# Kernel optimization log

Hardware: AMD Instinct MI355X
Metric: run time of the kernel (lower is better)

Reference implementation:

```python
import jax, jax.numpy as jnp
import numpy as np

EPS = 1e-5
ALPHA = 0.05   # propalpha
GDEP = 2       # gcn_depth
LAYERS = 3     # gcn_layers
NUM_TCN = 2    # num_layer tcn units per encoder


def conv1x1(W, b, x):
    # 1x1 Conv2d on [B,C,N,1]: pure channel mix
    return jnp.einsum('oc,bcnl->bonl', W, x) + b[None, :, None, None]


def tcn_unit(Wf, bf, Wg, bg, h):
    # gated TCN unit: tanh(filter) * sigmoid(gate), 1x1 convs (L==1)
    return jnp.tanh(conv1x1(Wf, bf, h)) * jax.nn.sigmoid(conv1x1(Wg, bg, h))


def mixprop(x, A, W, b):
    # MTGNN mixprop: add self-loops, row-normalize, gdep propagation steps,
    # concat hops on channel dim, 1x1 conv mlp. A: [N,N] or [B,N,N].
    N = A.shape[-1]
    A = A + jnp.eye(N, dtype=A.dtype)
    A = A / A.sum(-1, keepdims=True)
    h = x
    outs = [h]
    for _ in range(GDEP):
        if A.ndim == 2:
            hn = jnp.einsum('vw,bcwl->bcvl', A, h)
        else:
            hn = jnp.einsum('bvw,bcwl->bcvl', A, h)
        h = ALPHA * x + (1.0 - ALPHA) * hn
        outs.append(h)
    ho = jnp.concatenate(outs, axis=1)  # [B,(GDEP+1)*C,N,1]
    return conv1x1(W, b, ho)


def layernorm(x, w, b):
    # LayerNorm over (C,N,1) of [B,C,N,1]; idx=arange(N) selects full affine
    mu = x.mean(axis=(1, 2, 3), keepdims=True)
    var = x.var(axis=(1, 2, 3), keepdims=True)
    return (x - mu) / jnp.sqrt(var + EPS) * w[None] + b[None]


def setup_inputs() -> dict:
    key = jax.random.key(0)
    B, N, E, H, S, T = 8, 2048, 32, 128, 256, 12
    ks = jax.random.split(key, 32)
    s = 0.05
    inp = {
        'x': jax.random.normal(ks[0], (B, E, N, 1), jnp.float32),
        'dy_graph': jax.random.uniform(ks[1], (B, N, N), jnp.float32),
        'static_graph': jax.random.uniform(ks[2], (N, N), jnp.float32),
        'spatial_emb': jax.random.normal(ks[3], (B, 32, N, 1), jnp.float32),
        'temporal_d_emb': jax.random.normal(ks[4], (B, 32, N, 1), jnp.float32),
        'temporal_w_emb': jax.random.normal(ks[5], (B, 32, N, 1), jnp.float32),
        'enc_Wf': s * jax.random.normal(ks[6], (LAYERS, NUM_TCN, H, H), jnp.float32),
        'enc_bf': s * jax.random.normal(ks[7], (LAYERS, NUM_TCN, H), jnp.float32),
        'enc_Wg': s * jax.random.normal(ks[8], (LAYERS, NUM_TCN, H, H), jnp.float32),
        'enc_bg': s * jax.random.normal(ks[9], (LAYERS, NUM_TCN, H), jnp.float32),
        'skip_W': s * jax.random.normal(ks[10], (LAYERS, S, H), jnp.float32),
        'skip_b': s * jax.random.normal(ks[11], (LAYERS, S), jnp.float32),
        'norm_w': jnp.ones((LAYERS, E, N, 1), jnp.float32),
        'norm_b': jnp.zeros((LAYERS, E, N, 1), jnp.float32),
        'g0_W': s * jax.random.normal(ks[12], (LAYERS, E, (GDEP + 1) * E), jnp.float32),
        'g0_b': s * jax.random.normal(ks[13], (LAYERS, E), jnp.float32),
        'g1_W': s * jax.random.normal(ks[14], (LAYERS, E, (GDEP + 1) * E), jnp.float32),
        'g1_b': s * jax.random.normal(ks[15], (LAYERS, E), jnp.float32),
        'g2_W': s * jax.random.normal(ks[16], (LAYERS, E, (GDEP + 1) * E), jnp.float32),
        'g2_b': s * jax.random.normal(ks[17], (LAYERS, E), jnp.float32),
        'skipE_W': s * jax.random.normal(ks[18], (S, E), jnp.float32),
        'skipE_b': s * jax.random.normal(ks[19], (S,), jnp.float32),
        'end_W': s * jax.random.normal(ks[20], (T, S), jnp.float32),
        'end_b': s * jax.random.normal(ks[21], (T,), jnp.float32),
    }
    return inp


def reference(x, dy_graph, static_graph, spatial_emb, temporal_d_emb, temporal_w_emb,
              enc_Wf, enc_bf, enc_Wg, enc_bg, skip_W, skip_b, norm_w, norm_b,
              g0_W, g0_b, g1_W, g1_b, g2_W, g2_b, skipE_W, skipE_b, end_W, end_b):
    adp = dy_graph
    skip = 0.0
    for i in range(LAYERS):
        residual = x
        hidden = jnp.concatenate([x, spatial_emb, temporal_d_emb, temporal_w_emb], axis=1)
        for j in range(NUM_TCN):
            hidden = tcn_unit(enc_Wf[i, j], enc_bf[i, j], enc_Wg[i, j], enc_bg[i, j], hidden)
        skip = conv1x1(skip_W[i], skip_b[i], hidden) + skip
        x = (mixprop(x, static_graph, g0_W[i], g0_b[i])
             + mixprop(x, adp, g1_W[i], g1_b[i])
             + mixprop(x, jnp.swapaxes(adp, -1, -2), g2_W[i], g2_b[i]))
        x = x + residual
        x = jax.nn.relu(layernorm(x, norm_w[i], norm_b[i]))
    skip = conv1x1(skipE_W, skipE_b, x) + skip
    return conv1x1(end_W, end_b, skip)  # [B, seq_length, N, 1]
```

## Files before the change

### kernel.cpp

```cpp
#include <hip/hip_runtime.h>
#include <stdint.h>


typedef uint16_t u16;
typedef uint32_t u32;
typedef __attribute__((ext_vector_type(8))) short s8v;
typedef __attribute__((ext_vector_type(4))) float f4v;

#define MFMA16(a,b,c) __builtin_amdgcn_mfma_f32_16x16x32_bf16(a,b,c,0,0,0)

__device__ __forceinline__ float b2f(u16 u){ union{u32 i; float f;} x; x.i=(u32)u<<16; return x.f; }
__device__ __forceinline__ u16 f2b(float f){
  u32 u = __builtin_bit_cast(u32, f);
  u32 r = (u + 0x7fffu + ((u >> 16) & 1u)) >> 16;
  return (u16)r;
}

__device__ __forceinline__ void gld16(const void* g, void* l) {
  __builtin_amdgcn_global_load_lds(
      (const __attribute__((address_space(1))) void*)g,
      (__attribute__((address_space(3))) void*)l, 16, 0, 0);
}

__global__ __launch_bounds__(256) void kdetect(const u16* __restrict__ x, int* __restrict__ flag)
{
  const int i = blockIdx.x*256 + threadIdx.x;
  const uint4 v = ((const uint4*)x)[i];
  const u32 w[4] = {v.x, v.y, v.z, v.w};
  int cnt = 0;
  #pragma unroll
  for (int e = 0; e < 4; e++) {
    if ((w[e] & 0x7F80u) == 0x7F80u) cnt++;
    if (((w[e] >> 16) & 0x7F80u) == 0x7F80u) cnt++;
  }
  const unsigned long long m = __ballot(cnt != 0);
  if (m && (threadIdx.x & 63) == 0) atomicOr(flag, 1);
}

__global__ __launch_bounds__(256) void kcvt4(const void* __restrict__ src, u16* __restrict__ dst,
                                             int n4, const int* __restrict__ flag)
{
  if (!*flag) return;
  const int i = blockIdx.x*256 + threadIdx.x;
  if (i >= n4) return;
  const float4 v = ((const float4*)src)[i];
  u16 o[4]; o[0]=f2b(v.x); o[1]=f2b(v.y); o[2]=f2b(v.z); o[3]=f2b(v.w);
  *(uint2*)(dst + (long)i*4) = *(uint2*)o;
}

struct CvtTab { const void* s[18]; u16* d[18]; int n4[18]; };
__global__ __launch_bounds__(256) void kcvt_small(CvtTab tb, const int* __restrict__ flag)
{
  const int e = blockIdx.y;
  const int i = blockIdx.x*256 + threadIdx.x;
  if (i >= tb.n4[e]) return;
  if (*flag) {
    const float4 v = ((const float4*)tb.s[e])[i];
    u16 o[4]; o[0]=f2b(v.x); o[1]=f2b(v.y); o[2]=f2b(v.z); o[3]=f2b(v.w);
    *(uint2*)(tb.d[e] + (long)i*4) = *(uint2*)o;
  } else {
    *(uint2*)(tb.d[e] + (long)i*4) = ((const uint2*)tb.s[e])[i];
  }
}

__global__ __launch_bounds__(256) void kcvtT(
    const void* __restrict__ src, u16* __restrict__ dyb, u16* __restrict__ dytb,
    float* __restrict__ rsum, float* __restrict__ csum, const int* __restrict__ flag)
{
  __shared__ alignas(16) u32 tt[2][64][32];
  const int tid = threadIdx.x;
  const int b = blockIdx.z;
  const long r0 = (long)blockIdx.y*64;
  const long c0 = (long)blockIdx.x*128;
  const int rp = tid>>3, cg8 = (tid&7)*8;
  const long base = (long)b*4194304;
  const int fl = *flag;

  float rsl = 0.f, rsh = 0.f;
  #pragma unroll
  for (int h = 0; h < 2; h++) {
    u16 lo[8], hi[8];
    const long gl = base + (r0 + 2*rp)*2048 + c0 + h*64 + cg8;
    const long gh = gl + 2048;
    if (fl) {
      const float* sl = (const float*)src + gl;
      const float* sh = (const float*)src + gh;
      const float4 a0 = ((const float4*)sl)[0], a1 = ((const float4*)sl)[1];
      const float4 b0 = ((const float4*)sh)[0], b1 = ((const float4*)sh)[1];
      lo[0]=f2b(a0.x); lo[1]=f2b(a0.y); lo[2]=f2b(a0.z); lo[3]=f2b(a0.w);
      lo[4]=f2b(a1.x); lo[5]=f2b(a1.y); lo[6]=f2b(a1.z); lo[7]=f2b(a1.w);
      hi[0]=f2b(b0.x); hi[1]=f2b(b0.y); hi[2]=f2b(b0.z); hi[3]=f2b(b0.w);
      hi[4]=f2b(b1.x); hi[5]=f2b(b1.y); hi[6]=f2b(b1.z); hi[7]=f2b(b1.w);
      *(uint4*)(dyb + gl) = *(uint4*)lo;
      *(uint4*)(dyb + gh) = *(uint4*)hi;
    } else {
      *(uint4*)lo = *((const uint4*)((const u16*)src + gl));
      *(uint4*)hi = *((const uint4*)((const u16*)src + gh));
    }
    #pragma unroll
    for (int e = 0; e < 8; e++) {
      rsl += b2f(lo[e]); rsh += b2f(hi[e]);
      const int c = cg8 + e;
      tt[h][c][rp ^ ((c & 0x38) >> 1)] = (u32)lo[e] | ((u32)hi[e] << 16);
    }
  }
  rsl += __shfl_down(rsl, 4, 8); rsl += __shfl_down(rsl, 2, 8); rsl += __shfl_down(rsl, 1, 8);
  rsh += __shfl_down(rsh, 4, 8); rsh += __shfl_down(rsh, 2, 8); rsh += __shfl_down(rsh, 1, 8);
  if ((tid & 7) == 0) {
    atomicAdd(rsum + b*2048 + r0 + 2*rp,     rsl);
    atomicAdd(rsum + b*2048 + r0 + 2*rp + 1, rsh);
  }
  __syncthreads();

  #pragma unroll
  for (int h = 0; h < 2; h++) {
    const int c = tid>>2, j4 = (tid&3)*8;
    const int sw = (c & 0x38) >> 1;
    u32 q[8];
    *(uint4*)&q[0] = *(const uint4*)&tt[h][c][j4 ^ sw];
    *(uint4*)&q[4] = *(const uint4*)&tt[h][c][(j4 + 4) ^ sw];
    float cs = 0.f;
    #pragma unroll
    for (int e = 0; e < 8; e++) { cs += b2f((u16)q[e]); cs += b2f((u16)(q[e] >> 16)); }
    cs += __shfl_down(cs, 2, 4); cs += __shfl_down(cs, 1, 4);
    u16* dp = dytb + base + (c0 + h*64 + c)*2048 + r0 + 2*j4;
    *(uint4*)(dp)     = *(uint4*)&q[0];
    *(uint4*)(dp + 8) = *(uint4*)&q[4];
    if ((tid & 3) == 0) atomicAdd(csum + b*2048 + c0 + h*64 + c, cs);
  }
}

__global__ void kfin(float* __restrict__ v){
  const int i = blockIdx.x*256 + threadIdx.x;
  v[i] = 1.f/(1.f + v[i]);
}

struct PG {
  const u16* Ac0; const u16* Ac1; const u16* Ac2;
  const u16* Ar0; const u16* Ar1;
  const int* flag;
  long ab0, ab1, ab2;
  const u16* X0; const u16* X1; const u16* X2;
  const float* R0; const float* R1; const float* R2;
  long rb0, rb1, rb2;
  u16* O0; u16* O1; u16* O2;
};

__global__ __launch_bounds__(256) void kprops(PG p, long x_bs, long o_bs)
{
  __shared__ u16 Al[4][64][64];
  __shared__ u16 Xl[4][32][64];
  const int tid = threadIdx.x, wave = tid>>6, lane = tid&63;
  const int lw = lane&15, quad = lane>>4;
  const int wr = wave>>1, wc = wave&1;
  const int v0 = blockIdx.x*64;
  const int b = blockIdx.y, g = blockIdx.z;
  const int fl = *p.flag;
  const u16* Ag; long ab; const u16* Xg; const float* Rg; long rb; u16* Og;
  if (g == 0)      { Ag = fl ? p.Ac0 : p.Ar0; ab = p.ab0; Xg = p.X0; Rg = p.R0; rb = p.rb0; Og = p.O0; }
  else if (g == 1) { Ag = fl ? p.Ac1 : p.Ar1; ab = p.ab1; Xg = p.X1; Rg = p.R1; rb = p.rb1; Og = p.O1; }
  else             { Ag = p.Ac2;              ab = p.ab2; Xg = p.X2; Rg = p.R2; rb = p.rb2; Og = p.O2; }
  const u16* Ab = Ag + (long)b*ab;
  const u16* Xb = Xg + (long)b*x_bs;

  const int srow = wave*8 + (lane>>3);
  const int skc  = lane&7;
  const long soff = (long)((skc ^ (srow&7))*8);
  const u16* srcA0 = Ab + (long)(v0 + srow)*2048 + soff;
  const u16* srcA1 = Ab + (long)(v0 + 32 + srow)*2048 + soff;
  const u16* srcX  = Xb + (long)srow*2048 + soff;

#define STAGE(tt) do { const int bb_=(tt)&3; const long k0_=(long)(tt)*64;          \
    gld16(srcA0 + k0_, (void*)((char*)&Al[bb_][0][0]  + wave*1024));                \
    gld16(srcA1 + k0_, (void*)((char*)&Al[bb_][32][0] + wave*1024));                \
    gld16(srcX  + k0_, (void*)((char*)&Xl[bb_][0][0]  + wave*1024)); } while(0)

  f4v acc0 = {0.f,0.f,0.f,0.f}, acc1 = {0.f,0.f,0.f,0.f};
  const int arow0 = wr*32 + lw;
  const int arow1 = wr*32 + 16 + lw;
  const int xrow  = wc*16 + lw;
  const int sw    = lw & 7;
  const int q0    = (quad ^ sw)*8;
  const int q1    = ((quad ^ sw) ^ 4)*8;

  STAGE(0); STAGE(1); STAGE(2);

  #pragma unroll 1
  for (int t = 0; t < 32; t++) {
    if (t < 30)       asm volatile("s_waitcnt vmcnt(6)" ::: "memory");
    else if (t == 30) asm volatile("s_waitcnt vmcnt(3)" ::: "memory");
    else              asm volatile("s_waitcnt vmcnt(0)" ::: "memory");
    __builtin_amdgcn_s_barrier();
    __builtin_amdgcn_sched_barrier(0);
    const int bb = t&3;
    s8v x0  = *(const s8v*)&Xl[bb][xrow][q0];
    s8v a00 = *(const s8v*)&Al[bb][arow0][q0];
    s8v a10 = *(const s8v*)&Al[bb][arow1][q0];
    s8v x1  = *(const s8v*)&Xl[bb][xrow][q1];
    s8v a01 = *(const s8v*)&Al[bb][arow0][q1];
    s8v a11 = *(const s8v*)&Al[bb][arow1][q1];
    acc0 = MFMA16(a00, x0, acc0);
    acc1 = MFMA16(a10, x0, acc1);
    acc0 = MFMA16(a01, x1, acc0);
    acc1 = MFMA16(a11, x1, acc1);
    if (t <= 28) STAGE(t+3);
  }
#undef STAGE

  const int c = wc*16 + lw;
  const float* rp = Rg + (long)b*rb;
  u16* ob = Og + (long)b*o_bs;
  #pragma unroll
  for (int f = 0; f < 2; f++) {
    const f4v s = f ? acc1 : acc0;
    const int vb = v0 + wr*32 + f*16 + quad*4;
    const u16* dp = Xb + (long)c*2048 + vb;
    u16 pk[4];
    #pragma unroll
    for (int r = 0; r < 4; r++) pk[r] = f2b((s[r] + b2f(dp[r])) * rp[vb + r]);
    *(uint2*)(ob + (long)c*2048 + vb) = *(uint2*)pk;
  }
}

template<int TRANSA, int MODE>
__global__ __launch_bounds__(256) void kprop(
    const u16* __restrict__ A, long a_bs, int lda, int K,
    const u16* __restrict__ X, long x_bs, int ldx,
    const u16* __restrict__ D, long d_bs,
    const float* __restrict__ rinv, long r_bs,
    const float* __restrict__ bias,
    u16* __restrict__ out0, float* __restrict__ out1, long o_bs,
    float* __restrict__ stats)
{
  __shared__ u16 As[4][2][16][40];
  __shared__ f4v red[4][2][64];
  const int tid = threadIdx.x;
  const int wave = tid >> 6, lane = tid & 63;
  const int lw = lane & 15, quad = lane >> 4;
  const int v0 = blockIdx.x * 16;
  const int ball = blockIdx.z + blockIdx.y;
  const u16* Ab = A + (long)ball * a_bs;
  const u16* Xb = X + (long)ball * x_bs;
  const int KC = K >> 5;

  f4v acc0 = {0.f,0.f,0.f,0.f}, acc1 = {0.f,0.f,0.f,0.f};

  int r0, c0_;
  if (TRANSA == 0) { r0 = lane >> 2; c0_ = (lane & 3) * 8; }
  else             { r0 = lane >> 1; c0_ = (lane & 1) * 8; }

  int ci = wave;
  bool has = ci < KC;
  uint4 d = make_uint4(0,0,0,0);
  if (has) {
    d = (TRANSA == 0)
      ? *(const uint4*)(Ab + (long)(v0 + r0) * lda + ci * 32 + c0_)
      : *(const uint4*)(Ab + (long)(ci * 32 + r0) * lda + v0 + c0_);
  }
  int buf = 0;
  while (has) {
    if (TRANSA == 0) {
      *(uint4*)&As[wave][buf][r0][c0_] = d;
    } else {
      u16 tmp[8]; *(uint4*)tmp = d;
      #pragma unroll
      for (int e = 0; e < 8; e++) As[wave][buf][c0_ + e][r0] = tmp[e];
    }
    const int cn = ci + 4;
    const bool hn = cn < KC;
    if (hn) {
      d = (TRANSA == 0)
        ? *(const uint4*)(Ab + (long)(v0 + r0) * lda + cn * 32 + c0_)
        : *(const uint4*)(Ab + (long)(cn * 32 + r0) * lda + v0 + c0_);
    }
    s8v af = *(const s8v*)&As[wave][buf][lw][quad * 8];
    const u16* xk = Xb + ci * 32 + quad * 8;
    s8v b0 = *(const s8v*)(xk + (long)lw * ldx);
    s8v b1 = *(const s8v*)(xk + (long)(16 + lw) * ldx);
    acc0 = MFMA16(af, b0, acc0);
    acc1 = MFMA16(af, b1, acc1);
    ci = cn; has = hn; buf ^= 1;
  }
  red[wave][0][lane] = acc0;
  red[wave][1][lane] = acc1;
  __syncthreads();
  if (wave == 0) {
    const int vb = v0 + quad * 4;
    float ssum = 0.f, sq = 0.f;
    #pragma unroll
    for (int nt = 0; nt < 2; nt++) {
      f4v a = red[0][nt][lane] + red[1][nt][lane] + red[2][nt][lane] + red[3][nt][lane];
      const int c = nt * 16 + lw;
      const u16* dp = D + (long)ball * d_bs + (long)c * 2048 + vb;
      if (MODE == 0) {
        const float* rp = rinv + (long)ball * r_bs + vb;
        u16 pk[4];
        #pragma unroll
        for (int r = 0; r < 4; r++) pk[r] = f2b((a[r] + b2f(dp[r])) * rp[r]);
        *(uint2*)(out0 + (long)ball * o_bs + (long)c * 2048 + vb) = *(uint2*)pk;
      } else {
        const float bs = bias[c];
        float4 st;
        st.x = a[0] + bs + b2f(dp[0]);
        st.y = a[1] + bs + b2f(dp[1]);
        st.z = a[2] + bs + b2f(dp[2]);
        st.w = a[3] + bs + b2f(dp[3]);
        *(float4*)(out1 + (long)ball * o_bs + (long)c * 2048 + vb) = st;
        ssum += st.x + st.y + st.z + st.w;
        sq   += st.x*st.x + st.y*st.y + st.z*st.z + st.w*st.w;
      }
    }
    if (MODE == 1) {
      #pragma unroll
      for (int off = 32; off; off >>= 1) {
        ssum += __shfl_down(ssum, off, 64);
        sq   += __shfl_down(sq,   off, 64);
      }
      if (lane == 0) {
        atomicAdd(stats + ball*2,     ssum);
        atomicAdd(stats + ball*2 + 1, sq);
      }
    }
  }
}

__global__ __launch_bounds__(256) void ktcn(
    const u16* __restrict__ H, const u16* __restrict__ Wf, const u16* __restrict__ bfv,
    const u16* __restrict__ Wg, const u16* __restrict__ bgv, u16* __restrict__ out)
{
  const int tid = threadIdx.x, wave = tid>>6, lane = tid&63, lw = lane&15, quad = lane>>4;
  const long j0 = (long)blockIdx.x*64 + wave*16;
  const f4v zero = {0.f,0.f,0.f,0.f};
  f4v accf[8], accg[8];
  #pragma unroll
  for (int nt=0; nt<8; nt++){ accf[nt] = zero; accg[nt] = zero; }
  const u16* Arow = H + (j0 + lw)*128 + quad*8;
  #pragma unroll
  for (int k0 = 0; k0 < 128; k0 += 32) {
    s8v a = *(const s8v*)(Arow + k0);
    #pragma unroll
    for (int nt = 0; nt < 8; nt++) {
      const int o = nt*16 + lw;
      s8v bf_ = *(const s8v*)(Wf + o*128 + k0 + quad*8);
      s8v bg_ = *(const s8v*)(Wg + o*128 + k0 + quad*8);
      accf[nt] = MFMA16(a, bf_, accf[nt]);
      accg[nt] = MFMA16(a, bg_, accg[nt]);
    }
  }
  #pragma unroll
  for (int nt = 0; nt < 8; nt++) {
    const int o = nt*16 + lw;
    const float fb = b2f(bfv[o]), gb = b2f(bgv[o]);
    #pragma unroll
    for (int rr = 0; rr < 4; rr++) {
      const long j = j0 + quad*4 + rr;
      const float f = accf[nt][rr] + fb, g = accg[nt][rr] + gb;
      const float e2 = __expf(2.f*f);
      const float th = 1.f - 2.f/(e2 + 1.f);
      const float sg = 1.f/(1.f + __expf(-g));
      out[j*128 + o] = f2b(th*sg);
    }
  }
}

__global__ __launch_bounds__(256) void kskip(
    const u16* __restrict__ A, int lda, int K,
    const u16* __restrict__ W, int ldb,
    const u16* __restrict__ bias,
    float* __restrict__ skipbuf, int addprev, int mode, u16* __restrict__ outb)
{
  const int tid = threadIdx.x, wave = tid>>6, lane = tid&63, lw = lane&15, quad = lane>>4;
  const long j0 = (long)blockIdx.x*64 + wave*16;
  const f4v zero = {0.f,0.f,0.f,0.f};
  f4v acc[16];
  #pragma unroll
  for (int nt=0; nt<16; nt++) acc[nt] = zero;
  const u16* Arow = A + (j0 + lw)*(long)lda + quad*8;
  for (int k0 = 0; k0 < K; k0 += 32) {
    s8v a = *(const s8v*)(Arow + k0);
    #pragma unroll
    for (int nt = 0; nt < 16; nt++) {
      const int o = nt*16 + lw;
      s8v b = *(const s8v*)(W + (long)o*ldb + k0 + quad*8);
      acc[nt] = MFMA16(a, b, acc[nt]);
    }
  }
  #pragma unroll
  for (int nt = 0; nt < 16; nt++) {
    const int o = nt*16 + lw;
    const float bv = b2f(bias[o]);
    #pragma unroll
    for (int rr = 0; rr < 4; rr++) {
      const long j = j0 + quad*4 + rr;
      float v = acc[nt][rr] + bv;
      if (addprev) v += skipbuf[j*256 + o];
      if (mode == 0) skipbuf[j*256 + o] = v;
      else           outb[j*256 + o] = f2b(v);
    }
  }
}

__global__ __launch_bounds__(256) void kend(
    const u16* __restrict__ A, const u16* __restrict__ W, const u16* __restrict__ bias,
    void* __restrict__ outv, const int* __restrict__ flag)
{
  const int tid = threadIdx.x, wave = tid>>6, lane = tid&63, lw = lane&15, quad = lane>>4;
  const long j0 = (long)blockIdx.x*64 + wave*16;
  f4v acc = {0.f,0.f,0.f,0.f};
  const u16* Arow = A + (j0 + lw)*256 + quad*8;
  #pragma unroll
  for (int k0 = 0; k0 < 256; k0 += 32) {
    s8v a = *(const s8v*)(Arow + k0);
    s8v b = {0,0,0,0,0,0,0,0};
    if (lw < 12) b = *(const s8v*)(W + lw*256 + k0 + quad*8);
    acc = MFMA16(a, b, acc);
  }
  if (lw < 12) {
    const float bv = b2f(bias[lw]);
    const int fl = *flag;
    #pragma unroll
    for (int rr = 0; rr < 4; rr++) {
      const long j = j0 + quad*4 + rr;
      const long oi = (j >> 11)*24576 + lw*2048 + (j & 2047);
      const float val = acc[rr] + bv;
      if (fl) ((float*)outv)[oi] = val;
      else    ((u16*)outv)[oi]   = f2b(val);
    }
  }
}

__global__ __launch_bounds__(256) void khid0(
    const void* __restrict__ x, const void* __restrict__ spat,
    const void* __restrict__ tde, const void* __restrict__ twe,
    u16* __restrict__ hid, u16* __restrict__ slot0, const int* __restrict__ flag)
{
  __shared__ u16 t[32][72];
  const int tid = threadIdx.x, b = blockIdx.y, v0 = blockIdx.x*64;
  const int fl = *flag;
  const void* srcs[4] = {x, spat, tde, twe};
  #pragma unroll
  for (int e = 0; e < 4; e++) {
    const int c = tid>>3, v8 = (tid&7)*8;
    const long boff = (long)c*2048 + v0 + v8;
    u16 o8[8];
    if (fl) {
      const float* sp = (const float*)srcs[e] + (long)b*65536 + boff;
      const float4 a = ((const float4*)sp)[0], bb = ((const float4*)sp)[1];
      o8[0]=f2b(a.x); o8[1]=f2b(a.y); o8[2]=f2b(a.z); o8[3]=f2b(a.w);
      o8[4]=f2b(bb.x); o8[5]=f2b(bb.y); o8[6]=f2b(bb.z); o8[7]=f2b(bb.w);
    } else {
      *(uint4*)o8 = *(const uint4*)((const u16*)srcs[e] + (long)b*65536 + boff);
    }
    if (e == 0) *(uint4*)(slot0 + (long)b*458752 + boff) = *(uint4*)o8;
    *(uint4*)&t[c][v8] = *(uint4*)o8;
    __syncthreads();
    const int jl = tid>>2, c8 = (tid&3)*8;
    u16 q8[8];
    #pragma unroll
    for (int i = 0; i < 8; i++) q8[i] = t[c8 + i][jl];
    *(uint4*)(hid + ((long)b*2048 + v0 + jl)*128 + e*32 + c8) = *(uint4*)q8;
    __syncthreads();
  }
}

__global__ __launch_bounds__(256) void krowsum(const u16* __restrict__ srcA, const u16* __restrict__ srcB,
                                               const int* __restrict__ flag,
                                               float* __restrict__ outv, int nrows)
{
  const u16* src = (*flag) ? srcA : srcB;
  const int wave = threadIdx.x>>6, lane = threadIdx.x&63;
  const int row = blockIdx.x*4 + wave;
  if (row >= nrows) return;
  const u16* p = src + (long)row*2048 + lane*8;
  float s = 0.f;
  #pragma unroll
  for (int it = 0; it < 4; it++) {
    u16 v[8]; *(uint4*)v = *(const uint4*)(p + it*512);
    #pragma unroll
    for (int e = 0; e < 8; e++) s += b2f(v[e]);
  }
  #pragma unroll
  for (int off = 32; off; off >>= 1) s += __shfl_down(s, off, 64);
  if (lane == 0) outv[row] = 1.f/(1.f + s);
}

__global__ __launch_bounds__(256) void kweff(
    const u16* __restrict__ g0W, const u16* __restrict__ g1W, const u16* __restrict__ g2W,
    const u16* __restrict__ g0b, const u16* __restrict__ g1b, const u16* __restrict__ g2b,
    u16* __restrict__ weffA, float* __restrict__ bwA)
{
  const int L = blockIdx.y;
  const int ioff = L*3072, boff = L*32;
  u16* weff = weffA + L*7168;
  float* bw = bwA + L*32;
  const int idx = blockIdx.x*256 + threadIdx.x;
  if (idx < 32) bw[idx] = b2f(g0b[boff+idx]) + b2f(g1b[boff+idx]) + b2f(g2b[boff+idx]);
  if (idx >= 7168) return;
  const int o = idx / 224, m = idx % 224;
  const u16* Ws[3] = {g0W + ioff, g1W + ioff, g2W + ioff};
  float val;
  if (m < 32) {
    val = 0.f;
    #pragma unroll
    for (int g = 0; g < 3; g++) {
      const float w0 = b2f(Ws[g][o*96 + m]);
      const float w1 = b2f(Ws[g][o*96 + 32 + m]);
      const float w2 = b2f(Ws[g][o*96 + 64 + m]);
      val += w0 + 0.05f*(w1 + w2);
    }
  } else {
    const int f = (m - 32) >> 5, cc = m & 31;
    const int g = f >> 1, typ = f & 1;
    const float w1 = b2f(Ws[g][o*96 + 32 + cc]);
    const float w2 = b2f(Ws[g][o*96 + 64 + cc]);
    val = (typ == 0) ? (0.95f*w1 + 0.0475f*w2) : (0.9025f*w2);
  }
  weff[o*224 + m] = f2b(val);
}

__global__ __launch_bounds__(256) void kapply(
    const float* __restrict__ xpre, const float* __restrict__ raw,
    const u16* __restrict__ nw, const u16* __restrict__ nb,
    u16* __restrict__ slot0, u16* __restrict__ hid)
{
  __shared__ u16 t[32][72];
  const int tid = threadIdx.x, b = blockIdx.y, v0 = blockIdx.x*64;
  const float mu = raw[b*2] * (1.f/65536.f);
  const float var = raw[b*2+1] * (1.f/65536.f) - mu*mu;
  const float rs = rsqrtf(var + 1e-5f);
  const int c = tid>>3, v8 = (tid&7)*8;
  const long boff = (long)c*2048 + v0 + v8;
  float4 xa = *(const float4*)(xpre + (long)b*65536 + boff);
  float4 xbv = *(const float4*)(xpre + (long)b*65536 + boff + 4);
  u16 wv[8], bv[8], o8[8];
  *(uint4*)wv = *(const uint4*)(nw + boff);
  *(uint4*)bv = *(const uint4*)(nb + boff);
  const float xs[8] = {xa.x, xa.y, xa.z, xa.w, xbv.x, xbv.y, xbv.z, xbv.w};
  #pragma unroll
  for (int e = 0; e < 8; e++) {
    float y = (xs[e] - mu) * rs * b2f(wv[e]) + b2f(bv[e]);
    y = fmaxf(y, 0.f);
    o8[e] = f2b(y);
    t[c][v8 + e] = o8[e];
  }
  *(uint4*)(slot0 + (long)b*458752 + boff) = *(uint4*)o8;
  __syncthreads();
  const int jl = tid>>2, c8 = (tid&3)*8;
  u16 q8[8];
  #pragma unroll
  for (int e = 0; e < 8; e++) q8[e] = t[c8 + e][jl];
  *(uint4*)(hid + ((long)b*2048 + v0 + jl)*128 + c8) = *(uint4*)q8;
}

extern "C" void kernel_launch(void* const* d_in, const int* in_sizes, int n_in,
                              void* d_out, int out_size, void* d_ws, size_t ws_size,
                              hipStream_t stream)
{
  (void)in_sizes; (void)n_in; (void)out_size; (void)ws_size;

  char* ws = (char*)d_ws;
  u16*   pbuf = (u16*)(ws + 0);
  u16*   hid  = (u16*)(ws + 7340032);
  u16*   hb1  = (u16*)(ws + 11534336);
  u16*   hb2  = (u16*)(ws + 15728640);
  float* skip = (float*)(ws + 19922944);
  u16*   xsb  = (u16*)(ws + 36700160);
  float* xpre = (float*)(ws + 45088768);
  float* rst  = (float*)(ws + 47203328);
  float* rdy  = (float*)(ws + 47211520);
  float* cdy  = (float*)(ws + 47277056);
  int*   flag = (int*)(ws + 47343616);
  float* raw  = (float*)(ws + 47343744);

  size_t coff = 50331648;
  auto alloc = [&](size_t elems) -> u16* {
    u16* p = (u16*)(ws + coff);
    coff += ((elems*2 + 255)/256)*256;
    return p;
  };
  u16* dyb   = alloc(33554432);
  u16* stgb  = alloc(4194304);
  u16* encWf = alloc(98304);
  u16* encbf = alloc(768);
  u16* encWg = alloc(98304);
  u16* encbg = alloc(768);
  u16* skW   = alloc(98304);
  u16* skb   = alloc(768);
  u16* nw    = alloc(196608);
  u16* nb    = alloc(196608);
  u16* g0W   = alloc(9216);
  u16* g0b   = alloc(96);
  u16* g1W   = alloc(9216);
  u16* g1b   = alloc(96);
  u16* g2W   = alloc(9216);
  u16* g2b   = alloc(96);
  u16* sEW   = alloc(8192);
  u16* sEb   = alloc(256);
  u16* eW    = alloc(3072);
  u16* eb    = alloc(12);
  u16* dytb  = alloc(33554432);
  u16* weffA = alloc(21504);
  float* bwA = (float*)alloc(192);

  hipMemsetAsync(flag, 0, 320, stream);
  hipLaunchKernelGGL(kdetect, dim3(32), dim3(256), 0, stream, (const u16*)d_in[0], flag);

  CvtTab tb;
  {
    const void* ss[18] = { d_in[6], d_in[7], d_in[8], d_in[9], d_in[10], d_in[11],
      d_in[12], d_in[13], d_in[14], d_in[15], d_in[16], d_in[17], d_in[18], d_in[19],
      d_in[20], d_in[21], d_in[22], d_in[23] };
    u16* dd[18] = { encWf, encbf, encWg, encbg, skW, skb, nw, nb,
      g0W, g0b, g1W, g1b, g2W, g2b, sEW, sEb, eW, eb };
    const int nn[18] = { 24576, 192, 24576, 192, 24576, 192, 49152, 49152,
      2304, 24, 2304, 24, 2304, 24, 2048, 64, 768, 3 };
    for (int e = 0; e < 18; e++) { tb.s[e] = ss[e]; tb.d[e] = dd[e]; tb.n4[e] = nn[e]; }
  }
  hipLaunchKernelGGL(kcvt_small, dim3(192, 18), dim3(256), 0, stream, tb, flag);
  hipLaunchKernelGGL(kcvt4, dim3(4096), dim3(256), 0, stream, d_in[2], stgb, 1048576, flag);
  hipLaunchKernelGGL(kweff, dim3(28, 3), dim3(256), 0, stream,
      g0W, g1W, g2W, g0b, g1b, g2b, weffA, bwA);

  hipMemsetAsync(rdy, 0, 131072, stream);
  hipLaunchKernelGGL(kcvtT, dim3(16,32,8), dim3(256), 0, stream,
      d_in[1], dyb, dytb, rdy, cdy, flag);
  hipLaunchKernelGGL(kfin, dim3(128), dim3(256), 0, stream, rdy);
  hipLaunchKernelGGL(krowsum, dim3(512), dim3(256), 0, stream,
      stgb, (const u16*)d_in[2], flag, rst, 2048);
  hipLaunchKernelGGL(khid0, dim3(32,8), dim3(256), 0, stream,
      d_in[0], d_in[3], d_in[4], d_in[5], hid, pbuf, flag);

  const long PB = 458752;
  const long SL = 65536;
  const long DYB = 4194304;

  for (int i = 0; i < 3; i++) {
    hipLaunchKernelGGL(ktcn, dim3(256), dim3(256), 0, stream,
        hid, encWf + (i*2+0)*16384, encbf + (i*2+0)*128, encWg + (i*2+0)*16384, encbg + (i*2+0)*128, hb1);
    hipLaunchKernelGGL(ktcn, dim3(256), dim3(256), 0, stream,
        hb1, encWf + (i*2+1)*16384, encbf + (i*2+1)*128, encWg + (i*2+1)*16384, encbg + (i*2+1)*128, hb2);
    hipLaunchKernelGGL(kskip, dim3(256), dim3(256), 0, stream,
        hb2, 128, 128, skW + i*32768, 128, skb + i*256, skip, (i>0)?1:0, 0, (u16*)nullptr);

    PG p1;
    p1.Ac0 = stgb; p1.Ac1 = dyb; p1.Ac2 = dytb;
    p1.Ar0 = (const u16*)d_in[2]; p1.Ar1 = (const u16*)d_in[1];
    p1.flag = flag;
    p1.ab0 = 0;   p1.ab1 = DYB; p1.ab2 = DYB;
    p1.X0 = pbuf; p1.X1 = pbuf; p1.X2 = pbuf;
    p1.R0 = rst;  p1.R1 = rdy;  p1.R2 = cdy;
    p1.rb0 = 0;   p1.rb1 = 2048; p1.rb2 = 2048;
    p1.O0 = pbuf + 1*SL; p1.O1 = pbuf + 3*SL; p1.O2 = pbuf + 5*SL;
    hipLaunchKernelGGL(kprops, dim3(32,8,3), dim3(256), 0, stream, p1, PB, PB);

    PG p2 = p1;
    p2.X0 = pbuf + 1*SL; p2.X1 = pbuf + 3*SL; p2.X2 = pbuf + 5*SL;
    p2.O0 = pbuf + 2*SL; p2.O1 = pbuf + 4*SL; p2.O2 = pbuf + 6*SL;
    hipLaunchKernelGGL(kprops, dim3(32,8,3), dim3(256), 0, stream, p2, PB, PB);

    hipLaunchKernelGGL((kprop<1,1>), dim3(128,1,8), dim3(256), 0, stream,
        pbuf, PB, 2048, 224, weffA + i*7168, 0L, 224, pbuf, PB,
        (const float*)nullptr, 0L, bwA + i*32, (u16*)nullptr, xpre, 65536L, raw + i*16);
    hipLaunchKernelGGL(kapply, dim3(32,8), dim3(256), 0, stream,
        xpre, raw + i*16, nw + i*65536, nb + i*65536, pbuf, hid);
  }
  hipLaunchKernelGGL(kskip, dim3(256), dim3(256), 0, stream,
      hid, 128, 32, sEW, 32, sEb, skip, 1, 1, xsb);
  hipLaunchKernelGGL(kend, dim3(256), dim3(256), 0, stream, xsb, eW, eb, d_out, flag);
}
```

Before: 773.1 us.

## Fuse TCN and skip conv work into graph propagation launches as extra z-slices

The two gated TCN units are fused into one kernel that keeps the intermediate hidden tile in LDS, so the hb1 round trip through global memory goes away. That fused TCN runs as a fourth z-slice of the first propagation launch. The skip 1x1 conv becomes a fourth z-slice of the second propagation launch. This removes three launches per layer and lets the independent encoder work overlap with the memory-bound graph propagations. The cost is that the fused blocks share the propagation kernel's LDS allocation and register budget, which may lower occupancy for the prop blocks.

```diff
diff --git a/kernel.cpp b/kernel.cpp
--- a/kernel.cpp
+++ b/kernel.cpp
@@ -146,10 +146,10 @@
   u16* O0; u16* O1; u16* O2;
 };
 
-__global__ __launch_bounds__(256) void kprops(PG p, long x_bs, long o_bs)
-{
-  __shared__ u16 Al[4][64][64];
-  __shared__ u16 Xl[4][32][64];
+__device__ __forceinline__ void prop_body(
+    const PG& p, long x_bs, long o_bs,
+    u16 (&Al)[4][64][64], u16 (&Xl)[4][32][64])
+{
   const int tid = threadIdx.x, wave = tid>>6, lane = tid&63;
   const int lw = lane&15, quad = lane>>4;
   const int wr = wave>>1, wc = wave&1;
@@ -219,6 +219,127 @@
     #pragma unroll
     for (int r = 0; r < 4; r++) pk[r] = f2b((s[r] + b2f(dp[r])) * rp[vb + r]);
     *(uint2*)(ob + (long)c*2048 + vb) = *(uint2*)pk;
+  }
+}
+
+struct FR {
+  PG p;
+  const u16 *H, *Wf1, *bf1, *Wg1, *bg1, *Wf2, *bf2, *Wg2, *bg2;
+  u16* out;
+};
+
+__global__ __launch_bounds__(256) void kfront(FR f, long x_bs, long o_bs)
+{
+  __shared__ alignas(16) u16 Al[4][64][64];
+  __shared__ alignas(16) u16 Xl[4][32][64];
+  if (blockIdx.z < 3) { prop_body(f.p, x_bs, o_bs, Al, Xl); return; }
+
+  u16 (*h1)[16][136] = reinterpret_cast<u16 (*)[16][136]>(&Al[0][0][0]);
+  const int tid = threadIdx.x, wave = tid>>6, lane = tid&63, lw = lane&15, quad = lane>>4;
+  const int bid = blockIdx.y*32 + blockIdx.x;
+  const long j0 = (long)bid*64 + wave*16;
+  const f4v zero = {0.f,0.f,0.f,0.f};
+  f4v accf[8], accg[8];
+  #pragma unroll
+  for (int nt=0; nt<8; nt++){ accf[nt] = zero; accg[nt] = zero; }
+  const u16* Arow = f.H + (j0 + lw)*128 + quad*8;
+  #pragma unroll
+  for (int k0 = 0; k0 < 128; k0 += 32) {
+    s8v a = *(const s8v*)(Arow + k0);
+    #pragma unroll
+    for (int nt = 0; nt < 8; nt++) {
+      const int o = nt*16 + lw;
+      s8v bf_ = *(const s8v*)(f.Wf1 + o*128 + k0 + quad*8);
+      s8v bg_ = *(const s8v*)(f.Wg1 + o*128 + k0 + quad*8);
+      accf[nt] = MFMA16(a, bf_, accf[nt]);
+      accg[nt] = MFMA16(a, bg_, accg[nt]);
+    }
+  }
+  #pragma unroll
+  for (int nt = 0; nt < 8; nt++) {
+    const int o = nt*16 + lw;
+    const float fb = b2f(f.bf1[o]), gb = b2f(f.bg1[o]);
+    #pragma unroll
+    for (int rr = 0; rr < 4; rr++) {
+      const float ff = accf[nt][rr] + fb, gg = accg[nt][rr] + gb;
+      const float e2 = __expf(2.f*ff);
+      const float th = 1.f - 2.f/(e2 + 1.f);
+      const float sg = 1.f/(1.f + __expf(-gg));
+      h1[wave][quad*4 + rr][o] = f2b(th*sg);
+    }
+  }
+  __syncthreads();
+  #pragma unroll
+  for (int nt=0; nt<8; nt++){ accf[nt] = zero; accg[nt] = zero; }
+  #pragma unroll
+  for (int k0 = 0; k0 < 128; k0 += 32) {
+    s8v a = *(const s8v*)&h1[wave][lw][k0 + quad*8];
+    #pragma unroll
+    for (int nt = 0; nt < 8; nt++) {
+      const int o = nt*16 + lw;
+      s8v bf_ = *(const s8v*)(f.Wf2 + o*128 + k0 + quad*8);
+      s8v bg_ = *(const s8v*)(f.Wg2 + o*128 + k0 + quad*8);
+      accf[nt] = MFMA16(a, bf_, accf[nt]);
+      accg[nt] = MFMA16(a, bg_, accg[nt]);
+    }
+  }
+  #pragma unroll
+  for (int nt = 0; nt < 8; nt++) {
+    const int o = nt*16 + lw;
+    const float fb = b2f(f.bf2[o]), gb = b2f(f.bg2[o]);
+    #pragma unroll
+    for (int rr = 0; rr < 4; rr++) {
+      const long j = j0 + quad*4 + rr;
+      const float ff = accf[nt][rr] + fb, gg = accg[nt][rr] + gb;
+      const float e2 = __expf(2.f*ff);
+      const float th = 1.f - 2.f/(e2 + 1.f);
+      const float sg = 1.f/(1.f + __expf(-gg));
+      f.out[j*128 + o] = f2b(th*sg);
+    }
+  }
+}
+
+struct BK {
+  PG p;
+  const u16* A; const u16* W; const u16* bias;
+  float* skipbuf; int addprev;
+};
+
+__global__ __launch_bounds__(256) void kback(BK k, long x_bs, long o_bs)
+{
+  __shared__ alignas(16) u16 Al[4][64][64];
+  __shared__ alignas(16) u16 Xl[4][32][64];
+  if (blockIdx.z < 3) { prop_body(k.p, x_bs, o_bs, Al, Xl); return; }
+
+  const int tid = threadIdx.x, wave = tid>>6, lane = tid&63, lw = lane&15, quad = lane>>4;
+  const int bid = blockIdx.y*32 + blockIdx.x;
+  const long j0 = (long)bid*64 + wave*16;
+  const f4v zero = {0.f,0.f,0.f,0.f};
+  f4v acc[16];
+  #pragma unroll
+  for (int nt=0; nt<16; nt++) acc[nt] = zero;
+  const u16* Arow = k.A + (j0 + lw)*128 + quad*8;
+  #pragma unroll
+  for (int k0 = 0; k0 < 128; k0 += 32) {
+    s8v a = *(const s8v*)(Arow + k0);
+    #pragma unroll
+    for (int nt = 0; nt < 16; nt++) {
+      const int o = nt*16 + lw;
+      s8v b = *(const s8v*)(k.W + (long)o*128 + k0 + quad*8);
+      acc[nt] = MFMA16(a, b, acc[nt]);
+    }
+  }
+  #pragma unroll
+  for (int nt = 0; nt < 16; nt++) {
+    const int o = nt*16 + lw;
+    const float bv = b2f(k.bias[o]);
+    #pragma unroll
+    for (int rr = 0; rr < 4; rr++) {
+      const long j = j0 + quad*4 + rr;
+      float v = acc[nt][rr] + bv;
+      if (k.addprev) v += k.skipbuf[j*256 + o];
+      k.skipbuf[j*256 + o] = v;
+    }
   }
 }
 
@@ -324,45 +445,6 @@
   }
 }
 
-__global__ __launch_bounds__(256) void ktcn(
-    const u16* __restrict__ H, const u16* __restrict__ Wf, const u16* __restrict__ bfv,
-    const u16* __restrict__ Wg, const u16* __restrict__ bgv, u16* __restrict__ out)
-{
-  const int tid = threadIdx.x, wave = tid>>6, lane = tid&63, lw = lane&15, quad = lane>>4;
-  const long j0 = (long)blockIdx.x*64 + wave*16;
-  const f4v zero = {0.f,0.f,0.f,0.f};
-  f4v accf[8], accg[8];
-  #pragma unroll
-  for (int nt=0; nt<8; nt++){ accf[nt] = zero; accg[nt] = zero; }
-  const u16* Arow = H + (j0 + lw)*128 + quad*8;
-  #pragma unroll
-  for (int k0 = 0; k0 < 128; k0 += 32) {
-    s8v a = *(const s8v*)(Arow + k0);
-    #pragma unroll
-    for (int nt = 0; nt < 8; nt++) {
-      const int o = nt*16 + lw;
-      s8v bf_ = *(const s8v*)(Wf + o*128 + k0 + quad*8);
-      s8v bg_ = *(const s8v*)(Wg + o*128 + k0 + quad*8);
-      accf[nt] = MFMA16(a, bf_, accf[nt]);
-      accg[nt] = MFMA16(a, bg_, accg[nt]);
-    }
-  }
-  #pragma unroll
-  for (int nt = 0; nt < 8; nt++) {
-    const int o = nt*16 + lw;
-    const float fb = b2f(bfv[o]), gb = b2f(bgv[o]);
-    #pragma unroll
-    for (int rr = 0; rr < 4; rr++) {
-      const long j = j0 + quad*4 + rr;
-      const float f = accf[nt][rr] + fb, g = accg[nt][rr] + gb;
-      const float e2 = __expf(2.f*f);
-      const float th = 1.f - 2.f/(e2 + 1.f);
-      const float sg = 1.f/(1.f + __expf(-g));
-      out[j*128 + o] = f2b(th*sg);
-    }
-  }
-}
-
 __global__ __launch_bounds__(256) void kskip(
     const u16* __restrict__ A, int lda, int K,
     const u16* __restrict__ W, int ldb,
@@ -561,7 +643,6 @@
   char* ws = (char*)d_ws;
   u16*   pbuf = (u16*)(ws + 0);
   u16*   hid  = (u16*)(ws + 7340032);
-  u16*   hb1  = (u16*)(ws + 11534336);
   u16*   hb2  = (u16*)(ws + 15728640);
   float* skip = (float*)(ws + 19922944);
   u16*   xsb  = (u16*)(ws + 36700160);
@@ -635,13 +716,6 @@
   const long DYB = 4194304;
 
   for (int i = 0; i < 3; i++) {
-    hipLaunchKernelGGL(ktcn, dim3(256), dim3(256), 0, stream,
-        hid, encWf + (i*2+0)*16384, encbf + (i*2+0)*128, encWg + (i*2+0)*16384, encbg + (i*2+0)*128, hb1);
-    hipLaunchKernelGGL(ktcn, dim3(256), dim3(256), 0, stream,
-        hb1, encWf + (i*2+1)*16384, encbf + (i*2+1)*128, encWg + (i*2+1)*16384, encbg + (i*2+1)*128, hb2);
-    hipLaunchKernelGGL(kskip, dim3(256), dim3(256), 0, stream,
-        hb2, 128, 128, skW + i*32768, 128, skb + i*256, skip, (i>0)?1:0, 0, (u16*)nullptr);
-
     PG p1;
     p1.Ac0 = stgb; p1.Ac1 = dyb; p1.Ac2 = dytb;
     p1.Ar0 = (const u16*)d_in[2]; p1.Ar1 = (const u16*)d_in[1];
@@ -651,12 +725,24 @@
     p1.R0 = rst;  p1.R1 = rdy;  p1.R2 = cdy;
     p1.rb0 = 0;   p1.rb1 = 2048; p1.rb2 = 2048;
     p1.O0 = pbuf + 1*SL; p1.O1 = pbuf + 3*SL; p1.O2 = pbuf + 5*SL;
-    hipLaunchKernelGGL(kprops, dim3(32,8,3), dim3(256), 0, stream, p1, PB, PB);
-
-    PG p2 = p1;
-    p2.X0 = pbuf + 1*SL; p2.X1 = pbuf + 3*SL; p2.X2 = pbuf + 5*SL;
-    p2.O0 = pbuf + 2*SL; p2.O1 = pbuf + 4*SL; p2.O2 = pbuf + 6*SL;
-    hipLaunchKernelGGL(kprops, dim3(32,8,3), dim3(256), 0, stream, p2, PB, PB);
+
+    FR fr;
+    fr.p = p1;
+    fr.H = hid;
+    fr.Wf1 = encWf + (i*2+0)*16384; fr.bf1 = encbf + (i*2+0)*128;
+    fr.Wg1 = encWg + (i*2+0)*16384; fr.bg1 = encbg + (i*2+0)*128;
+    fr.Wf2 = encWf + (i*2+1)*16384; fr.bf2 = encbf + (i*2+1)*128;
+    fr.Wg2 = encWg + (i*2+1)*16384; fr.bg2 = encbg + (i*2+1)*128;
+    fr.out = hb2;
+    hipLaunchKernelGGL(kfront, dim3(32,8,4), dim3(256), 0, stream, fr, PB, PB);
+
+    BK bk;
+    bk.p = p1;
+    bk.p.X0 = pbuf + 1*SL; bk.p.X1 = pbuf + 3*SL; bk.p.X2 = pbuf + 5*SL;
+    bk.p.O0 = pbuf + 2*SL; bk.p.O1 = pbuf + 4*SL; bk.p.O2 = pbuf + 6*SL;
+    bk.A = hb2; bk.W = skW + i*32768; bk.bias = skb + i*256;
+    bk.skipbuf = skip; bk.addprev = (i>0)?1:0;
+    hipLaunchKernelGGL(kback, dim3(32,8,4), dim3(256), 0, stream, bk, PB, PB);
 
     hipLaunchKernelGGL((kprop<1,1>), dim3(128,1,8), dim3(256), 0, stream,
         pbuf, PB, 2048, 224, weffA + i*7168, 0L, 224, pbuf, PB,
```

Result: slower. 791.1 us (+2.3%).
